# Kernel tuning notes

Measured on AMD Instinct MI355X. Metric: run time of the kernel, lower is better.

Reference implementation:

```python
import jax, jax.numpy as jnp
import numpy as np

N = 50000      # nodes
E = 800000     # edges (before self loops)
G = 64         # graphs in batch
F_IN = 11
HID = 64
C = 8
NEG_SLOPE = 0.2


def setup_inputs() -> dict:
    key = jax.random.key(0)
    ks = jax.random.split(key, 20)
    inp = {
        "x": jax.random.normal(ks[0], (N, F_IN), dtype=jnp.float32),
        "edge_index": jax.random.randint(ks[1], (2, E), 0, N, dtype=jnp.int64),
        "edge_attr": jax.random.normal(ks[2], (E, 17), dtype=jnp.float32),
        "batch": jnp.sort(jax.random.randint(ks[3], (N,), 0, G, dtype=jnp.int64)),
    }
    def glorot(k, shape):
        fan_in, fan_out = shape[0], shape[-1]
        s = jnp.sqrt(6.0 / (fan_in + fan_out))
        return jax.random.uniform(k, shape, jnp.float32, -s, s)
    # GATConv layers (heads=1): W [in,out], att vectors a_src/a_dst [out], bias [out]
    inp["W1"] = glorot(ks[4], (F_IN, HID)); inp["a1s"] = glorot(ks[5], (HID,)); inp["a1d"] = glorot(ks[6], (HID,)); inp["b1"] = jnp.zeros((HID,), jnp.float32)
    inp["W2"] = glorot(ks[7], (HID, HID)); inp["a2s"] = glorot(ks[8], (HID,)); inp["a2d"] = glorot(ks[9], (HID,)); inp["b2"] = jnp.zeros((HID,), jnp.float32)
    inp["W3"] = glorot(ks[10], (HID, C)); inp["a3s"] = glorot(ks[11], (C,)); inp["a3d"] = glorot(ks[12], (C,)); inp["b3"] = jnp.zeros((C,), jnp.float32)
    return inp


def _gat_layer(x, src, dst, W, a_s, a_d, b):
    # x: [N,in] -> h: [N,out]; single head, concat irrelevant for heads=1
    h = x @ W
    alpha_src = h @ a_s            # [N]
    alpha_dst = h @ a_d            # [N]
    e = jax.nn.leaky_relu(alpha_src[src] + alpha_dst[dst], negative_slope=NEG_SLOPE)  # [E']
    # segment-wise (per destination node) softmax over incoming edges
    m = jax.ops.segment_max(e, dst, num_segments=N)
    ex = jnp.exp(e - m[dst])
    denom = jax.ops.segment_sum(ex, dst, num_segments=N)
    alpha = ex / denom[dst]
    out = jax.ops.segment_sum(alpha[:, None] * h[src], dst, num_segments=N)
    return out + b


def reference(x, edge_index, edge_attr, batch, W1, a1s, a1d, b1, W2, a2s, a2d, b2, W3, a3s, a3d, b3):
    del edge_attr  # GATConv without edge_dim ignores edge_attr
    loop = jnp.arange(N, dtype=edge_index.dtype)
    src = jnp.concatenate([edge_index[0], loop])  # add self loops
    dst = jnp.concatenate([edge_index[1], loop])
    h = jax.nn.relu(_gat_layer(x, src, dst, W1, a1s, a1d, b1))
    h = jax.nn.relu(_gat_layer(h, src, dst, W2, a2s, a2d, b2))
    h = jax.nn.relu(_gat_layer(h, src, dst, W3, a3s, a3d, b3))
    # global mean pool over graphs
    counts = jax.ops.segment_sum(jnp.ones((N,), h.dtype), batch, num_segments=G)
    pooled = jax.ops.segment_sum(h, batch, num_segments=G) / jnp.maximum(counts, 1.0)[:, None]
    # dropout is identity in eval mode
    return jax.nn.sigmoid(pooled)
```

## Files before the change

kernel.cpp:

```cpp
#include <hip/hip_runtime.h>

#define NN 50000
#define EE 800000
#define GG 64
#define CC 8

#define NBKT 196
#define NCHK 782
#define CHUNK 1024
#define CAP 8192
#define NB4G 12500

__device__ unsigned g_done = 0;

__device__ __forceinline__ float lrelu(float z) { return fmaxf(z, 0.2f * z); }
__device__ __forceinline__ unsigned short f2bf(float v) {
    unsigned u = __float_as_uint(v);
    return (unsigned short)((u + 0x7FFFu + ((u >> 16) & 1u)) >> 16);
}
__device__ __forceinline__ float bf2f(unsigned short b) {
    return __uint_as_float(((unsigned)b) << 16);
}
__device__ __forceinline__ float2 bf2x2(unsigned d) {
    float2 r;
    r.x = __uint_as_float(d << 16);
    r.y = __uint_as_float(d & 0xFFFF0000u);
    return r;
}


__global__ __launch_bounds__(256) void k0_mm11_hist(const float* __restrict__ x, const float* __restrict__ W,
                                                    const float* __restrict__ avs, const float* __restrict__ avd,
                                                    unsigned short* __restrict__ h, float* __restrict__ as_,
                                                    float* __restrict__ ad_, const int* __restrict__ dst,
                                                    int* __restrict__ G) {
    __shared__ float xT[11 * 68];
    __shared__ float Wl[11 * 64];
    __shared__ float avl[64], adl[64];
    __shared__ int hist[NBKT];
    int t = threadIdx.x;
    int nbase = blockIdx.x * 64;
    for (int idx = t; idx < 11 * 64; idx += 256) Wl[idx] = W[idx];
    if (t < 64) { avl[t] = avs[t]; adl[t] = avd[t]; }
    for (int idx = t; idx < 64 * 11; idx += 256) {
        int n = idx / 11, k = idx - n * 11;
        int gn = nbase + n;
        if (gn >= NN) gn = NN - 1;
        xT[k * 68 + n] = x[gn * 11 + k];
    }
    for (int i = t; i < NBKT; i += 256) hist[i] = 0;
    __syncthreads();
    int f0 = (t & 15) * 4;
    int n0 = (t >> 4) * 4;
    float a00=0,a01=0,a02=0,a03=0, a10=0,a11=0,a12=0,a13=0;
    float a20=0,a21=0,a22=0,a23=0, a30=0,a31=0,a32=0,a33=0;
#pragma unroll
    for (int k = 0; k < 11; k++) {
        float4 xv = *(const float4*)&xT[k * 68 + n0];
        float4 wv = *(const float4*)&Wl[k * 64 + f0];
        a00 += xv.x * wv.x; a01 += xv.x * wv.y; a02 += xv.x * wv.z; a03 += xv.x * wv.w;
        a10 += xv.y * wv.x; a11 += xv.y * wv.y; a12 += xv.y * wv.z; a13 += xv.y * wv.w;
        a20 += xv.z * wv.x; a21 += xv.z * wv.y; a22 += xv.z * wv.z; a23 += xv.z * wv.w;
        a30 += xv.w * wv.x; a31 += xv.w * wv.y; a32 += xv.w * wv.z; a33 += xv.w * wv.w;
    }
    float4 av = *(const float4*)&avl[f0];
    float4 dv = *(const float4*)&adl[f0];
    float vs[4], vd[4];
    vs[0] = a00*av.x + a01*av.y + a02*av.z + a03*av.w;
    vs[1] = a10*av.x + a11*av.y + a12*av.z + a13*av.w;
    vs[2] = a20*av.x + a21*av.y + a22*av.z + a23*av.w;
    vs[3] = a30*av.x + a31*av.y + a32*av.z + a33*av.w;
    vd[0] = a00*dv.x + a01*dv.y + a02*dv.z + a03*dv.w;
    vd[1] = a10*dv.x + a11*dv.y + a12*dv.z + a13*dv.w;
    vd[2] = a20*dv.x + a21*dv.y + a22*dv.z + a23*dv.w;
    vd[3] = a30*dv.x + a31*dv.y + a32*dv.z + a33*dv.w;
#pragma unroll
    for (int o = 1; o < 16; o <<= 1) {
#pragma unroll
        for (int ni = 0; ni < 4; ni++) {
            vs[ni] += __shfl_xor(vs[ni], o);
            vd[ni] += __shfl_xor(vd[ni], o);
        }
    }
    ushort4* h4 = (ushort4*)h;
    int nn0 = nbase + n0;
    float rows[4][4] = {{a00,a01,a02,a03},{a10,a11,a12,a13},{a20,a21,a22,a23},{a30,a31,a32,a33}};
#pragma unroll
    for (int ni = 0; ni < 4; ni++) {
        if (nn0 + ni < NN) {
            ushort4 pv;
            pv.x = f2bf(rows[ni][0]); pv.y = f2bf(rows[ni][1]);
            pv.z = f2bf(rows[ni][2]); pv.w = f2bf(rows[ni][3]);
            h4[(nn0 + ni) * 16 + (t & 15)] = pv;
            if ((t & 15) == 0) { as_[nn0 + ni] = vs[ni]; ad_[nn0 + ni] = vd[ni]; }
        }
    }
    int e0 = blockIdx.x * CHUNK;
    int e1 = min(e0 + CHUNK, EE);
    for (int e = e0 + t; e < e1; e += 256) atomicAdd(&hist[dst[e] >> 8], 1);
    __syncthreads();
    for (int i = t; i < NBKT; i += 256) G[blockIdx.x * NBKT + i] = hist[i];
}


__global__ __launch_bounds__(256) void k1_scan(const int* __restrict__ G, int* __restrict__ offs,
                                               int* __restrict__ bT, float* __restrict__ pool,
                                               float* __restrict__ cntf, int* __restrict__ rowptr) {
    __shared__ int s[256];
    int t = threadIdx.x, j = blockIdx.x;
    int c0 = t * 4;
    int v0 = (c0 + 0 < NCHK) ? G[(c0 + 0) * NBKT + j] : 0;
    int v1 = (c0 + 1 < NCHK) ? G[(c0 + 1) * NBKT + j] : 0;
    int v2 = (c0 + 2 < NCHK) ? G[(c0 + 2) * NBKT + j] : 0;
    int v3 = (c0 + 3 < NCHK) ? G[(c0 + 3) * NBKT + j] : 0;
    int tsum = v0 + v1 + v2 + v3;
    s[t] = tsum;
    __syncthreads();
#pragma unroll
    for (int off = 1; off < 256; off <<= 1) {
        int u = (t >= off) ? s[t - off] : 0;
        __syncthreads();
        s[t] += u;
        __syncthreads();
    }
    int excl = s[t] - tsum;
    if (c0 + 0 < NCHK) offs[(c0 + 0) * NBKT + j] = excl;
    if (c0 + 1 < NCHK) offs[(c0 + 1) * NBKT + j] = excl + v0;
    if (c0 + 2 < NCHK) offs[(c0 + 2) * NBKT + j] = excl + v0 + v1;
    if (c0 + 3 < NCHK) offs[(c0 + 3) * NBKT + j] = excl + v0 + v1 + v2;
    if (t == 255) bT[j] = s[255];
    if (j == 0) {
        for (int i = t; i < GG * CC; i += 256) pool[i] = 0.f;
        if (t < GG) cntf[t] = 0.f;
        if (t == 0) rowptr[NN] = EE;
    }
}


__global__ __launch_bounds__(256) void k2_part(const int* __restrict__ src, const int* __restrict__ dst,
                                               const int* __restrict__ offs, const int* __restrict__ bT,
                                               unsigned* __restrict__ pairs) {
    __shared__ int s[256];
    __shared__ int bst[NBKT];
    __shared__ int cur[NBKT];
    int t = threadIdx.x, c = blockIdx.x;
    int v = (t < NBKT) ? bT[t] : 0;
    s[t] = v;
    __syncthreads();
#pragma unroll
    for (int off = 1; off < 256; off <<= 1) {
        int u = (t >= off) ? s[t - off] : 0;
        __syncthreads();
        s[t] += u;
        __syncthreads();
    }
    if (t < NBKT) bst[t] = s[t] - v;
    __syncthreads();
    for (int i = t; i < NBKT; i += 256) cur[i] = bst[i] + offs[c * NBKT + i];
    __syncthreads();
    int e0 = c * CHUNK, e1 = min(e0 + CHUNK, EE);
    for (int e = e0 + t; e < e1; e += 256) {
        int d = dst[e];
        int pos = atomicAdd(&cur[d >> 8], 1);
        pairs[pos] = (unsigned)src[e] | ((unsigned)(d & 255) << 16);
    }
}


__global__ __launch_bounds__(256) void k3_sort(const unsigned* __restrict__ pairs, const int* __restrict__ bT,
                                               int* __restrict__ col, int* __restrict__ rowptr) {
    __shared__ unsigned pL[CAP];
    __shared__ int hist[256];
    __shared__ int sc[256];
    int t = threadIdx.x, j = blockIdx.x;
    int v = (t < NBKT) ? bT[t] : 0;
    hist[t] = v;
    __syncthreads();
#pragma unroll
    for (int off = 1; off < 256; off <<= 1) {
        int u = (t >= off) ? hist[t - off] : 0;
        __syncthreads();
        hist[t] += u;
        __syncthreads();
    }
    if (t == j) { sc[0] = hist[t] - v; sc[1] = v; }
    __syncthreads();
    int start = sc[0];
    int cnt = sc[1];
    if (cnt > CAP) cnt = CAP;
    int nb = j * 256;
    int nodeCnt = min(256, NN - nb);
    __syncthreads();
    hist[t] = 0;
    __syncthreads();
    for (int i = t; i < cnt; i += 256) {
        unsigned p = pairs[start + i];
        pL[i] = p;
        atomicAdd(&hist[p >> 16], 1);
    }
    __syncthreads();
    int c2 = hist[t];
    sc[t] = c2;
    __syncthreads();
#pragma unroll
    for (int off = 1; off < 256; off <<= 1) {
        int u = (t >= off) ? sc[t - off] : 0;
        __syncthreads();
        sc[t] += u;
        __syncthreads();
    }
    int excl = sc[t] - c2;
    if (t < nodeCnt) rowptr[nb + t] = start + excl;
    hist[t] = excl;
    __syncthreads();
    for (int i = t; i < cnt; i += 256) {
        unsigned p = pL[i];
        int pos = atomicAdd(&hist[p >> 16], 1);
        col[start + pos] = (int)(p & 0xFFFFu);
    }
}


__global__ __launch_bounds__(256) void k_mm64t(const unsigned short* __restrict__ xin,
                                               const float* __restrict__ W,
                                               const float* __restrict__ avs, const float* __restrict__ avd,
                                               unsigned short* __restrict__ h, float* __restrict__ as_,
                                               float* __restrict__ ad_) {
    __shared__ float xT[64 * 68];
    __shared__ float Wl[64 * 64];
    __shared__ float avl[64], adl[64];
    int t = threadIdx.x;
    int nbase = blockIdx.x * 64;
    for (int idx = t; idx < 64 * 64; idx += 256) Wl[idx] = W[idx];
    if (t < 64) { avl[t] = avs[t]; adl[t] = avd[t]; }
    for (int idx = t; idx < 64 * 64; idx += 256) {
        int n = idx / 64, k = idx - n * 64;
        int gn = nbase + n;
        if (gn >= NN) gn = NN - 1;
        xT[k * 68 + n] = bf2f(xin[gn * 64 + k]);
    }
    __syncthreads();
    int f0 = (t & 15) * 4;
    int n0 = (t >> 4) * 4;
    float a00=0,a01=0,a02=0,a03=0, a10=0,a11=0,a12=0,a13=0;
    float a20=0,a21=0,a22=0,a23=0, a30=0,a31=0,a32=0,a33=0;
#pragma unroll 4
    for (int k = 0; k < 64; k++) {
        float4 xv = *(const float4*)&xT[k * 68 + n0];
        float4 wv = *(const float4*)&Wl[k * 64 + f0];
        a00 += xv.x * wv.x; a01 += xv.x * wv.y; a02 += xv.x * wv.z; a03 += xv.x * wv.w;
        a10 += xv.y * wv.x; a11 += xv.y * wv.y; a12 += xv.y * wv.z; a13 += xv.y * wv.w;
        a20 += xv.z * wv.x; a21 += xv.z * wv.y; a22 += xv.z * wv.z; a23 += xv.z * wv.w;
        a30 += xv.w * wv.x; a31 += xv.w * wv.y; a32 += xv.w * wv.z; a33 += xv.w * wv.w;
    }
    float4 av = *(const float4*)&avl[f0];
    float4 dv = *(const float4*)&adl[f0];
    float vs[4], vd[4];
    vs[0] = a00*av.x + a01*av.y + a02*av.z + a03*av.w;
    vs[1] = a10*av.x + a11*av.y + a12*av.z + a13*av.w;
    vs[2] = a20*av.x + a21*av.y + a22*av.z + a23*av.w;
    vs[3] = a30*av.x + a31*av.y + a32*av.z + a33*av.w;
    vd[0] = a00*dv.x + a01*dv.y + a02*dv.z + a03*dv.w;
    vd[1] = a10*dv.x + a11*dv.y + a12*dv.z + a13*dv.w;
    vd[2] = a20*dv.x + a21*dv.y + a22*dv.z + a23*dv.w;
    vd[3] = a30*dv.x + a31*dv.y + a32*dv.z + a33*dv.w;
#pragma unroll
    for (int o = 1; o < 16; o <<= 1) {
#pragma unroll
        for (int ni = 0; ni < 4; ni++) {
            vs[ni] += __shfl_xor(vs[ni], o);
            vd[ni] += __shfl_xor(vd[ni], o);
        }
    }
    ushort4* h4 = (ushort4*)h;
    int nn0 = nbase + n0;
    float rows[4][4] = {{a00,a01,a02,a03},{a10,a11,a12,a13},{a20,a21,a22,a23},{a30,a31,a32,a33}};
#pragma unroll
    for (int ni = 0; ni < 4; ni++) {
        if (nn0 + ni < NN) {
            ushort4 pv;
            pv.x = f2bf(rows[ni][0]); pv.y = f2bf(rows[ni][1]);
            pv.z = f2bf(rows[ni][2]); pv.w = f2bf(rows[ni][3]);
            h4[(nn0 + ni) * 16 + (t & 15)] = pv;
            if ((t & 15) == 0) { as_[nn0 + ni] = vs[ni]; ad_[nn0 + ni] = vd[ni]; }
        }
    }
}


template <bool FUSE>
__global__ __launch_bounds__(256) void k_agg64(const unsigned short* __restrict__ h,
                                               const int* __restrict__ rowptr,
                                               const int* __restrict__ col, const float* __restrict__ as_,
                                               const float* __restrict__ ad_, const float* __restrict__ bias,
                                               unsigned short* __restrict__ out16,
                                               const float* __restrict__ W3, const float* __restrict__ a3s,
                                               const float* __restrict__ a3d,
                                               float* __restrict__ as3, float* __restrict__ ad3) {
    __shared__ float W3p[64 * 9];
    if constexpr (FUSE) {
        for (int idx = threadIdx.x; idx < 512; idx += 256)
            W3p[(idx >> 3) * 9 + (idx & 7)] = W3[idx];
        __syncthreads();
    }
    int wid = threadIdx.x >> 6;
    int node = blockIdx.x * 4 + wid;
    int lane = threadIdx.x & 63;
    int rp0 = rowptr[node];
    int deg = rowptr[node + 1] - rp0;
    float adn = ad_[node];
    float zself = lrelu(as_[node] + adn);
    const uint4* hb4 = (const uint4*)h;
    int f = lane & 7, eg = lane >> 3;
    float acc[8] = {0.f, 0.f, 0.f, 0.f, 0.f, 0.f, 0.f, 0.f};
    if (deg <= 32) {
        uint4 rowreg[4];
        float zk[4];
#pragma unroll
        for (int k = 0; k < 4; k++) {
            int e = k * 8 + eg;
            zk[k] = -1e30f;
            if (e < deg) {
                int se = col[rp0 + e];
                zk[k] = lrelu(as_[se] + adn);
                rowreg[k] = hb4[se * 8 + f];
            }
        }
        float M = fmaxf(fmaxf(zk[0], zk[1]), fmaxf(zk[2], zk[3]));
#pragma unroll
        for (int o = 8; o <= 32; o <<= 1) M = fmaxf(M, __shfl_xor(M, o));
        M = fmaxf(M, zself);
        float s0 = 0.f;
#pragma unroll
        for (int k = 0; k < 4; k++) { zk[k] = __expf(zk[k] - M); s0 += zk[k]; }
        float exs = __expf(zself - M);
        float sum = s0;
#pragma unroll
        for (int o = 8; o <= 32; o <<= 1) sum += __shfl_xor(sum, o);
        float inv = 1.f / (sum + exs);
#pragma unroll
        for (int k = 0; k < 4; k++) {
            int e = k * 8 + eg;
            if (e < deg) {
                float w = zk[k] * inv;
                float2 p0 = bf2x2(rowreg[k].x), p1 = bf2x2(rowreg[k].y);
                float2 p2 = bf2x2(rowreg[k].z), p3 = bf2x2(rowreg[k].w);
                acc[0] += w * p0.x; acc[1] += w * p0.y;
                acc[2] += w * p1.x; acc[3] += w * p1.y;
                acc[4] += w * p2.x; acc[5] += w * p2.y;
                acc[6] += w * p3.x; acc[7] += w * p3.y;
            }
        }
        if (eg == 0) {
            float w0 = exs * inv;
            uint4 hv = hb4[node * 8 + f];
            float2 p0 = bf2x2(hv.x), p1 = bf2x2(hv.y), p2 = bf2x2(hv.z), p3 = bf2x2(hv.w);
            acc[0] += w0 * p0.x; acc[1] += w0 * p0.y;
            acc[2] += w0 * p1.x; acc[3] += w0 * p1.y;
            acc[4] += w0 * p2.x; acc[5] += w0 * p2.y;
            acc[6] += w0 * p3.x; acc[7] += w0 * p3.y;
        }
    } else {
        float m = -1e30f, l = 0.f;
        for (int i = lane; i < deg; i += 64) {
            float z = lrelu(as_[col[rp0 + i]] + adn);
            float mn = fmaxf(m, z);
            l = l * __expf(m - mn) + __expf(z - mn);
            m = mn;
        }
        if (lane == 0) {
            float mn = fmaxf(m, zself);
            l = l * __expf(m - mn) + __expf(zself - mn);
            m = mn;
        }
#pragma unroll
        for (int o = 32; o; o >>= 1) {
            float mo = __shfl_xor(m, o), lo = __shfl_xor(l, o);
            float mn = fmaxf(m, mo);
            l = l * __expf(m - mn) + lo * __expf(mo - mn);
            m = mn;
        }
        float Em = m;
        float inv = 1.f / l;
        for (int base = 0; base < deg; base += 8) {
            int i = base + eg;
            if (i < deg) {
                int sv = col[rp0 + i];
                float al = __expf(lrelu(as_[sv] + adn) - Em) * inv;
                uint4 hv = hb4[sv * 8 + f];
                float2 p0 = bf2x2(hv.x), p1 = bf2x2(hv.y), p2 = bf2x2(hv.z), p3 = bf2x2(hv.w);
                acc[0] += al * p0.x; acc[1] += al * p0.y;
                acc[2] += al * p1.x; acc[3] += al * p1.y;
                acc[4] += al * p2.x; acc[5] += al * p2.y;
                acc[6] += al * p3.x; acc[7] += al * p3.y;
            }
        }
        if (eg == 0) {
            float al = __expf(zself - Em) * inv;
            uint4 hv = hb4[node * 8 + f];
            float2 p0 = bf2x2(hv.x), p1 = bf2x2(hv.y), p2 = bf2x2(hv.z), p3 = bf2x2(hv.w);
            acc[0] += al * p0.x; acc[1] += al * p0.y;
            acc[2] += al * p1.x; acc[3] += al * p1.y;
            acc[4] += al * p2.x; acc[5] += al * p2.y;
            acc[6] += al * p3.x; acc[7] += al * p3.y;
        }
    }
#pragma unroll
    for (int o = 8; o <= 32; o <<= 1) {
#pragma unroll
        for (int j = 0; j < 8; j++) acc[j] += __shfl_xor(acc[j], o);
    }
    float4 b0 = ((const float4*)bias)[2 * f];
    float4 b1 = ((const float4*)bias)[2 * f + 1];
    float r[8];
    r[0] = fmaxf(acc[0] + b0.x, 0.f); r[1] = fmaxf(acc[1] + b0.y, 0.f);
    r[2] = fmaxf(acc[2] + b0.z, 0.f); r[3] = fmaxf(acc[3] + b0.w, 0.f);
    r[4] = fmaxf(acc[4] + b1.x, 0.f); r[5] = fmaxf(acc[5] + b1.y, 0.f);
    r[6] = fmaxf(acc[6] + b1.z, 0.f); r[7] = fmaxf(acc[7] + b1.w, 0.f);
    if constexpr (!FUSE) {
        if (eg == 0) {
            uint4 pv;
            pv.x = (unsigned)f2bf(r[0]) | ((unsigned)f2bf(r[1]) << 16);
            pv.y = (unsigned)f2bf(r[2]) | ((unsigned)f2bf(r[3]) << 16);
            pv.z = (unsigned)f2bf(r[4]) | ((unsigned)f2bf(r[5]) << 16);
            pv.w = (unsigned)f2bf(r[6]) | ((unsigned)f2bf(r[7]) << 16);
            ((uint4*)out16)[node * 8 + f] = pv;
        }
    } else {
        float p = 0.f;
#pragma unroll
        for (int i = 0; i < 8; i++) p += r[i] * W3p[(f * 8 + i) * 9 + eg];
#pragma unroll
        for (int o = 1; o < 8; o <<= 1) p += __shfl_xor(p, o);
        float vs = p * a3s[eg];
        float vd = p * a3d[eg];
#pragma unroll
        for (int o = 8; o <= 32; o <<= 1) { vs += __shfl_xor(vs, o); vd += __shfl_xor(vd, o); }
        if (lane == 0) { as3[node] = vs; ad3[node] = vd; }
        if (f == 0) out16[node * 8 + eg] = f2bf(p);
    }
}


__global__ __launch_bounds__(256) void k_agg8(const unsigned short* __restrict__ h,
                                              const int* __restrict__ rowptr,
                                              const int* __restrict__ col, const float* __restrict__ as_,
                                              const float* __restrict__ ad_, const float* __restrict__ bias,
                                              float* __restrict__ out) {
    int wid = threadIdx.x >> 6;
    int node = blockIdx.x * 4 + wid;
    int lane = threadIdx.x & 63;
    int rp0 = rowptr[node];
    int deg = rowptr[node + 1] - rp0;
    float adn = ad_[node];
    float zself = lrelu(as_[node] + adn);
    const uint2* h2 = (const uint2*)h;
    int f = lane & 1, eg = lane >> 1;
    float acc[4] = {0.f, 0.f, 0.f, 0.f};
    if (deg <= 32) {
        float z = -1e30f;
        uint2 rr = make_uint2(0u, 0u);
        if (eg < deg) {
            int se = col[rp0 + eg];
            z = lrelu(as_[se] + adn);
            rr = h2[se * 2 + f];
        }
        float M = z;
#pragma unroll
        for (int o = 2; o <= 32; o <<= 1) M = fmaxf(M, __shfl_xor(M, o));
        M = fmaxf(M, zself);
        float ex = __expf(z - M);
        float exs = __expf(zself - M);
        float sum = ex;
#pragma unroll
        for (int o = 2; o <= 32; o <<= 1) sum += __shfl_xor(sum, o);
        float inv = 1.f / (sum + exs);
        float w = ex * inv;
        float2 lo = bf2x2(rr.x), hi = bf2x2(rr.y);
        acc[0] = w * lo.x; acc[1] = w * lo.y; acc[2] = w * hi.x; acc[3] = w * hi.y;
        if (eg == 0) {
            float w0 = exs * inv;
            uint2 hv = h2[node * 2 + f];
            float2 l2 = bf2x2(hv.x), h2v = bf2x2(hv.y);
            acc[0] += w0 * l2.x; acc[1] += w0 * l2.y;
            acc[2] += w0 * h2v.x; acc[3] += w0 * h2v.y;
        }
    } else {
        float m = -1e30f, l = 0.f;
        for (int i = lane; i < deg; i += 64) {
            float z = lrelu(as_[col[rp0 + i]] + adn);
            float mn = fmaxf(m, z);
            l = l * __expf(m - mn) + __expf(z - mn);
            m = mn;
        }
        if (lane == 0) {
            float mn = fmaxf(m, zself);
            l = l * __expf(m - mn) + __expf(zself - mn);
            m = mn;
        }
#pragma unroll
        for (int o = 32; o; o >>= 1) {
            float mo = __shfl_xor(m, o), lo = __shfl_xor(l, o);
            float mn = fmaxf(m, mo);
            l = l * __expf(m - mn) + lo * __expf(mo - mn);
            m = mn;
        }
        float Em = m;
        float inv = 1.f / l;
        for (int base = 0; base < deg; base += 32) {
            int i = base + eg;
            if (i < deg) {
                int sv = col[rp0 + i];
                float al = __expf(lrelu(as_[sv] + adn) - Em) * inv;
                uint2 hv = h2[sv * 2 + f];
                float2 lo = bf2x2(hv.x), hi = bf2x2(hv.y);
                acc[0] += al * lo.x; acc[1] += al * lo.y;
                acc[2] += al * hi.x; acc[3] += al * hi.y;
            }
        }
        if (eg == 0) {
            float al = __expf(zself - Em) * inv;
            uint2 hv = h2[node * 2 + f];
            float2 lo = bf2x2(hv.x), hi = bf2x2(hv.y);
            acc[0] += al * lo.x; acc[1] += al * lo.y;
            acc[2] += al * hi.x; acc[3] += al * hi.y;
        }
    }
#pragma unroll
    for (int o = 2; o <= 32; o <<= 1) {
#pragma unroll
        for (int j = 0; j < 4; j++) acc[j] += __shfl_xor(acc[j], o);
    }
    if (eg == 0) {
        float4 bv = ((const float4*)bias)[f];
        float4 o4;
        o4.x = fmaxf(acc[0] + bv.x, 0.f);
        o4.y = fmaxf(acc[1] + bv.y, 0.f);
        o4.z = fmaxf(acc[2] + bv.z, 0.f);
        o4.w = fmaxf(acc[3] + bv.w, 0.f);
        ((float4*)out)[node * 2 + f] = o4;
    }
}


__global__ __launch_bounds__(256) void k9_poolfinal(const float* __restrict__ h3, const int* __restrict__ batch,
                                                    float* __restrict__ pool, float* __restrict__ cntf,
                                                    float* __restrict__ out) {
    __shared__ float pl[GG * CC + GG];
    __shared__ int lastFlag;
    int t = threadIdx.x;
    for (int idx = t; idx < GG * CC + GG; idx += 256) pl[idx] = 0.f;
    __syncthreads();
    int node = blockIdx.x * 256 + t;
    if (node < NN) {
        int g = batch[node];
#pragma unroll
        for (int c = 0; c < CC; c++) atomicAdd(&pl[g * CC + c], h3[node * CC + c]);
        atomicAdd(&pl[GG * CC + g], 1.0f);
    }
    __syncthreads();
    for (int idx = t; idx < GG * CC + GG; idx += 256) {
        float v = pl[idx];
        if (idx < GG * CC)
            atomicAdd(&pool[idx], v);
        else
            atomicAdd(&cntf[idx - GG * CC], v);
    }
    __syncthreads();
    if (t == 0) {
        __threadfence();
        unsigned r = __hip_atomic_fetch_add(&g_done, 1u, __ATOMIC_ACQ_REL, __HIP_MEMORY_SCOPE_AGENT);
        lastFlag = (r == (unsigned)(NBKT - 1));
    }
    __syncthreads();
    if (lastFlag) {
        __threadfence();
        for (int i = t; i < GG * CC; i += 256) {
            int g = i >> 3;
            float c = __hip_atomic_load(&cntf[g], __ATOMIC_RELAXED, __HIP_MEMORY_SCOPE_AGENT);
            float p = __hip_atomic_load(&pool[i], __ATOMIC_RELAXED, __HIP_MEMORY_SCOPE_AGENT);
            float v = p / fmaxf(c, 1.0f);
            out[i] = 1.0f / (1.0f + __expf(-v));
        }
        if (t == 0)
            __hip_atomic_store(&g_done, 0u, __ATOMIC_RELAXED, __HIP_MEMORY_SCOPE_AGENT);
    }
}


extern "C" void kernel_launch(void* const* d_in, const int* in_sizes, int n_in,
                              void* d_out, int out_size, void* d_ws, size_t ws_size,
                              hipStream_t stream) {
    const float* x   = (const float*)d_in[0];
    const int*   ei  = (const int*)d_in[1];
    const int*   bat = (const int*)d_in[3];
    const float* W1  = (const float*)d_in[4];
    const float* a1s = (const float*)d_in[5];
    const float* a1d = (const float*)d_in[6];
    const float* b1  = (const float*)d_in[7];
    const float* W2  = (const float*)d_in[8];
    const float* a2s = (const float*)d_in[9];
    const float* a2d = (const float*)d_in[10];
    const float* b2  = (const float*)d_in[11];
    const float* W3  = (const float*)d_in[12];
    const float* a3s = (const float*)d_in[13];
    const float* a3d = (const float*)d_in[14];
    const float* b3  = (const float*)d_in[15];
    float* out = (float*)d_out;

    float* fb = (float*)d_ws;
    unsigned short* hA16 = (unsigned short*)fb;
    unsigned short* hB16 = (unsigned short*)(fb + NN * 32);
    unsigned short* h316 = (unsigned short*)(fb + NN * 64);
    float* h3b  = fb + NN * 64 + NN * 4;
    float* as_  = h3b + NN * 8;
    float* ad_  = as_ + NN;
    float* as3  = ad_ + NN;
    float* ad3  = as3 + NN;
    int* rowptr = (int*)(ad3 + NN);
    int* col    = rowptr + NN + 1;
    int* G      = col + EE;
    int* offs   = G + NCHK * NBKT;
    int* bT     = offs + NCHK * NBKT;
    unsigned* pairs = (unsigned*)(bT + 256);
    float* pool = (float*)(pairs + EE);
    float* cntf = pool + GG * CC;

    const int NB64 = (NN + 63) / 64;

    const int* srcE = ei;
    const int* dstE = ei + EE;

    k0_mm11_hist<<<NB64, 256, 0, stream>>>(x, W1, a1s, a1d, hA16, as_, ad_, dstE, G);
    k1_scan<<<NBKT, 256, 0, stream>>>(G, offs, bT, pool, cntf, rowptr);
    k2_part<<<NCHK, 256, 0, stream>>>(srcE, dstE, offs, bT, pairs);
    k3_sort<<<NBKT, 256, 0, stream>>>(pairs, bT, col, rowptr);

    k_agg64<false><<<NB4G, 256, 0, stream>>>(hA16, rowptr, col, as_, ad_, b1, hB16,
                                             nullptr, nullptr, nullptr, nullptr, nullptr);
    k_mm64t<<<NB64, 256, 0, stream>>>(hB16, W2, a2s, a2d, hA16, as_, ad_);
    k_agg64<true><<<NB4G, 256, 0, stream>>>(hA16, rowptr, col, as_, ad_, b2, h316,
                                            W3, a3s, a3d, as3, ad3);
    k_agg8<<<NB4G, 256, 0, stream>>>(h316, rowptr, col, as3, ad3, b3, h3b);
    k9_poolfinal<<<NBKT, 256, 0, stream>>>(h3b, bat, pool, cntf, out);
}
```

Measured before the change: 268.6 us.

## Build CSR with per-node global atomic counts and direct scatter instead of bucket sort

Replaces the two-level bucket partition plus in-LDS sort with a simpler CSR build. Per-destination counts come from global atomics, then a two-pass block scan and a global-atomic scatter of source indices into col. This drops the pairs buffer, the per-chunk histogram matrix and the LDS sort kernel. In exchange it adds heavy contended global atomics and a non-deterministic edge order within each row, which can change floating-point summation order.

Result: slower. 324.8 us (+20.9%).

```diff
diff --git a/kernel.cpp b/kernel.cpp
--- a/kernel.cpp
+++ b/kernel.cpp
@@ -8,8 +8,8 @@
 #define NBKT 196
 #define NCHK 782
 #define CHUNK 1024
-#define CAP 8192
 #define NB4G 12500
+#define NBE  3125
 
 __device__ unsigned g_done = 0;
 
@@ -29,15 +29,25 @@
 }
 
 
+__global__ __launch_bounds__(256) void k_init(int* __restrict__ cnt, float* __restrict__ pool,
+                                              float* __restrict__ cntf) {
+    int n = blockIdx.x * 256 + threadIdx.x;
+    if (n < NN) cnt[n] = 0;
+    if (blockIdx.x == 0) {
+        for (int i = threadIdx.x; i < GG * CC; i += 256) pool[i] = 0.f;
+        if (threadIdx.x < GG) cntf[threadIdx.x] = 0.f;
+    }
+}
+
+
 __global__ __launch_bounds__(256) void k0_mm11_hist(const float* __restrict__ x, const float* __restrict__ W,
                                                     const float* __restrict__ avs, const float* __restrict__ avd,
                                                     unsigned short* __restrict__ h, float* __restrict__ as_,
                                                     float* __restrict__ ad_, const int* __restrict__ dst,
-                                                    int* __restrict__ G) {
+                                                    int* __restrict__ cnt) {
     __shared__ float xT[11 * 68];
     __shared__ float Wl[11 * 64];
     __shared__ float avl[64], adl[64];
-    __shared__ int hist[NBKT];
     int t = threadIdx.x;
     int nbase = blockIdx.x * 64;
     for (int idx = t; idx < 11 * 64; idx += 256) Wl[idx] = W[idx];
@@ -48,7 +58,6 @@
         if (gn >= NN) gn = NN - 1;
         xT[k * 68 + n] = x[gn * 11 + k];
     }
-    for (int i = t; i < NBKT; i += 256) hist[i] = 0;
     __syncthreads();
     int f0 = (t & 15) * 4;
     int n0 = (t >> 4) * 4;
@@ -97,24 +106,17 @@
     }
     int e0 = blockIdx.x * CHUNK;
     int e1 = min(e0 + CHUNK, EE);
-    for (int e = e0 + t; e < e1; e += 256) atomicAdd(&hist[dst[e] >> 8], 1);
-    __syncthreads();
-    for (int i = t; i < NBKT; i += 256) G[blockIdx.x * NBKT + i] = hist[i];
-}
-
-
-__global__ __launch_bounds__(256) void k1_scan(const int* __restrict__ G, int* __restrict__ offs,
-                                               int* __restrict__ bT, float* __restrict__ pool,
-                                               float* __restrict__ cntf, int* __restrict__ rowptr) {
+    for (int e = e0 + t; e < e1; e += 256) atomicAdd(&cnt[dst[e]], 1);
+}
+
+
+__global__ __launch_bounds__(256) void k1a_scan(const int* __restrict__ cnt, int* __restrict__ rowptr,
+                                                int* __restrict__ bsum) {
     __shared__ int s[256];
     int t = threadIdx.x, j = blockIdx.x;
-    int c0 = t * 4;
-    int v0 = (c0 + 0 < NCHK) ? G[(c0 + 0) * NBKT + j] : 0;
-    int v1 = (c0 + 1 < NCHK) ? G[(c0 + 1) * NBKT + j] : 0;
-    int v2 = (c0 + 2 < NCHK) ? G[(c0 + 2) * NBKT + j] : 0;
-    int v3 = (c0 + 3 < NCHK) ? G[(c0 + 3) * NBKT + j] : 0;
-    int tsum = v0 + v1 + v2 + v3;
-    s[t] = tsum;
+    int n = j * 256 + t;
+    int v = (n < NN) ? cnt[n] : 0;
+    s[t] = v;
     __syncthreads();
 #pragma unroll
     for (int off = 1; off < 256; off <<= 1) {
@@ -123,100 +125,39 @@
         s[t] += u;
         __syncthreads();
     }
-    int excl = s[t] - tsum;
-    if (c0 + 0 < NCHK) offs[(c0 + 0) * NBKT + j] = excl;
-    if (c0 + 1 < NCHK) offs[(c0 + 1) * NBKT + j] = excl + v0;
-    if (c0 + 2 < NCHK) offs[(c0 + 2) * NBKT + j] = excl + v0 + v1;
-    if (c0 + 3 < NCHK) offs[(c0 + 3) * NBKT + j] = excl + v0 + v1 + v2;
-    if (t == 255) bT[j] = s[255];
-    if (j == 0) {
-        for (int i = t; i < GG * CC; i += 256) pool[i] = 0.f;
-        if (t < GG) cntf[t] = 0.f;
-        if (t == 0) rowptr[NN] = EE;
-    }
-}
-
-
-__global__ __launch_bounds__(256) void k2_part(const int* __restrict__ src, const int* __restrict__ dst,
-                                               const int* __restrict__ offs, const int* __restrict__ bT,
-                                               unsigned* __restrict__ pairs) {
+    if (n < NN) rowptr[n] = s[t] - v;
+    if (t == 255) bsum[j] = s[255];
+}
+
+__global__ __launch_bounds__(256) void k1b_add(int* __restrict__ rowptr, const int* __restrict__ bsum,
+                                               int* __restrict__ cursor) {
     __shared__ int s[256];
-    __shared__ int bst[NBKT];
-    __shared__ int cur[NBKT];
-    int t = threadIdx.x, c = blockIdx.x;
-    int v = (t < NBKT) ? bT[t] : 0;
-    s[t] = v;
-    __syncthreads();
-#pragma unroll
-    for (int off = 1; off < 256; off <<= 1) {
-        int u = (t >= off) ? s[t - off] : 0;
+    int t = threadIdx.x, j = blockIdx.x;
+    s[t] = (t < j) ? bsum[t] : 0;
+    __syncthreads();
+#pragma unroll
+    for (int off = 128; off; off >>= 1) {
+        if (t < off) s[t] += s[t + off];
         __syncthreads();
-        s[t] += u;
-        __syncthreads();
-    }
-    if (t < NBKT) bst[t] = s[t] - v;
-    __syncthreads();
-    for (int i = t; i < NBKT; i += 256) cur[i] = bst[i] + offs[c * NBKT + i];
-    __syncthreads();
-    int e0 = c * CHUNK, e1 = min(e0 + CHUNK, EE);
-    for (int e = e0 + t; e < e1; e += 256) {
+    }
+    int offset = s[0];
+    int n = j * 256 + t;
+    if (n < NN) {
+        int r = rowptr[n] + offset;
+        rowptr[n] = r;
+        cursor[n] = r;
+    }
+    if (j == 0 && t == 0) rowptr[NN] = EE;
+}
+
+
+__global__ __launch_bounds__(256) void k2s_scatter(const int* __restrict__ src, const int* __restrict__ dst,
+                                                   int* __restrict__ cursor, int* __restrict__ col) {
+    int e = blockIdx.x * 256 + threadIdx.x;
+    if (e < EE) {
         int d = dst[e];
-        int pos = atomicAdd(&cur[d >> 8], 1);
-        pairs[pos] = (unsigned)src[e] | ((unsigned)(d & 255) << 16);
-    }
-}
-
-
-__global__ __launch_bounds__(256) void k3_sort(const unsigned* __restrict__ pairs, const int* __restrict__ bT,
-                                               int* __restrict__ col, int* __restrict__ rowptr) {
-    __shared__ unsigned pL[CAP];
-    __shared__ int hist[256];
-    __shared__ int sc[256];
-    int t = threadIdx.x, j = blockIdx.x;
-    int v = (t < NBKT) ? bT[t] : 0;
-    hist[t] = v;
-    __syncthreads();
-#pragma unroll
-    for (int off = 1; off < 256; off <<= 1) {
-        int u = (t >= off) ? hist[t - off] : 0;
-        __syncthreads();
-        hist[t] += u;
-        __syncthreads();
-    }
-    if (t == j) { sc[0] = hist[t] - v; sc[1] = v; }
-    __syncthreads();
-    int start = sc[0];
-    int cnt = sc[1];
-    if (cnt > CAP) cnt = CAP;
-    int nb = j * 256;
-    int nodeCnt = min(256, NN - nb);
-    __syncthreads();
-    hist[t] = 0;
-    __syncthreads();
-    for (int i = t; i < cnt; i += 256) {
-        unsigned p = pairs[start + i];
-        pL[i] = p;
-        atomicAdd(&hist[p >> 16], 1);
-    }
-    __syncthreads();
-    int c2 = hist[t];
-    sc[t] = c2;
-    __syncthreads();
-#pragma unroll
-    for (int off = 1; off < 256; off <<= 1) {
-        int u = (t >= off) ? sc[t - off] : 0;
-        __syncthreads();
-        sc[t] += u;
-        __syncthreads();
-    }
-    int excl = sc[t] - c2;
-    if (t < nodeCnt) rowptr[nb + t] = start + excl;
-    hist[t] = excl;
-    __syncthreads();
-    for (int i = t; i < cnt; i += 256) {
-        unsigned p = pL[i];
-        int pos = atomicAdd(&hist[p >> 16], 1);
-        col[start + pos] = (int)(p & 0xFFFFu);
+        int pos = atomicAdd(&cursor[d], 1);
+        col[pos] = src[e];
     }
 }
 
@@ -619,11 +560,10 @@
     float* ad3  = as3 + NN;
     int* rowptr = (int*)(ad3 + NN);
     int* col    = rowptr + NN + 1;
-    int* G      = col + EE;
-    int* offs   = G + NCHK * NBKT;
-    int* bT     = offs + NCHK * NBKT;
-    unsigned* pairs = (unsigned*)(bT + 256);
-    float* pool = (float*)(pairs + EE);
+    int* cnt    = col + EE;
+    int* cursor = cnt + NN;
+    int* bsum   = cursor + NN;
+    float* pool = (float*)(bsum + 256);
     float* cntf = pool + GG * CC;
 
     const int NB64 = (NN + 63) / 64;
@@ -631,10 +571,11 @@
     const int* srcE = ei;
     const int* dstE = ei + EE;
 
-    k0_mm11_hist<<<NB64, 256, 0, stream>>>(x, W1, a1s, a1d, hA16, as_, ad_, dstE, G);
-    k1_scan<<<NBKT, 256, 0, stream>>>(G, offs, bT, pool, cntf, rowptr);
-    k2_part<<<NCHK, 256, 0, stream>>>(srcE, dstE, offs, bT, pairs);
-    k3_sort<<<NBKT, 256, 0, stream>>>(pairs, bT, col, rowptr);
+    k_init<<<NBKT, 256, 0, stream>>>(cnt, pool, cntf);
+    k0_mm11_hist<<<NB64, 256, 0, stream>>>(x, W1, a1s, a1d, hA16, as_, ad_, dstE, cnt);
+    k1a_scan<<<NBKT, 256, 0, stream>>>(cnt, rowptr, bsum);
+    k1b_add<<<NBKT, 256, 0, stream>>>(rowptr, bsum, cursor);
+    k2s_scatter<<<NBE, 256, 0, stream>>>(srcE, dstE, cursor, col);
 
     k_agg64<false><<<NB4G, 256, 0, stream>>>(hA16, rowptr, col, as_, ad_, b1, hB16,
                                              nullptr, nullptr, nullptr, nullptr, nullptr);
```

## Fuse layer-2 linear transform into layer-1 aggregation epilogue

Applied to the files above, without the earlier changes.

Removes the standalone 64x64 matmul kernel and computes h@W2 plus the attention logits inside the layer-1 aggregation kernel, once each node's aggregated row is ready. The intermediate bf16 activation no longer makes a separate write-then-read round trip, and one launch is dropped. In exchange, each block stages a transposed 64x66 W2 tile in shared memory. Each wavefront also does extra FMAs and shuffle reductions per node, which may lower occupancy and lengthen the aggregation kernel. Separate as2/ad2 buffers are added so the next layer does not read the logits being overwritten.

Result: slower. 309.1 us (+15.1%).

```diff
diff --git a/kernel.cpp b/kernel.cpp
--- a/kernel.cpp
+++ b/kernel.cpp
@@ -221,91 +221,34 @@
 }
 
 
-__global__ __launch_bounds__(256) void k_mm64t(const unsigned short* __restrict__ xin,
-                                               const float* __restrict__ W,
-                                               const float* __restrict__ avs, const float* __restrict__ avd,
-                                               unsigned short* __restrict__ h, float* __restrict__ as_,
-                                               float* __restrict__ ad_) {
-    __shared__ float xT[64 * 68];
-    __shared__ float Wl[64 * 64];
-    __shared__ float avl[64], adl[64];
-    int t = threadIdx.x;
-    int nbase = blockIdx.x * 64;
-    for (int idx = t; idx < 64 * 64; idx += 256) Wl[idx] = W[idx];
-    if (t < 64) { avl[t] = avs[t]; adl[t] = avd[t]; }
-    for (int idx = t; idx < 64 * 64; idx += 256) {
-        int n = idx / 64, k = idx - n * 64;
-        int gn = nbase + n;
-        if (gn >= NN) gn = NN - 1;
-        xT[k * 68 + n] = bf2f(xin[gn * 64 + k]);
-    }
-    __syncthreads();
-    int f0 = (t & 15) * 4;
-    int n0 = (t >> 4) * 4;
-    float a00=0,a01=0,a02=0,a03=0, a10=0,a11=0,a12=0,a13=0;
-    float a20=0,a21=0,a22=0,a23=0, a30=0,a31=0,a32=0,a33=0;
-#pragma unroll 4
-    for (int k = 0; k < 64; k++) {
-        float4 xv = *(const float4*)&xT[k * 68 + n0];
-        float4 wv = *(const float4*)&Wl[k * 64 + f0];
-        a00 += xv.x * wv.x; a01 += xv.x * wv.y; a02 += xv.x * wv.z; a03 += xv.x * wv.w;
-        a10 += xv.y * wv.x; a11 += xv.y * wv.y; a12 += xv.y * wv.z; a13 += xv.y * wv.w;
-        a20 += xv.z * wv.x; a21 += xv.z * wv.y; a22 += xv.z * wv.z; a23 += xv.z * wv.w;
-        a30 += xv.w * wv.x; a31 += xv.w * wv.y; a32 += xv.w * wv.z; a33 += xv.w * wv.w;
-    }
-    float4 av = *(const float4*)&avl[f0];
-    float4 dv = *(const float4*)&adl[f0];
-    float vs[4], vd[4];
-    vs[0] = a00*av.x + a01*av.y + a02*av.z + a03*av.w;
-    vs[1] = a10*av.x + a11*av.y + a12*av.z + a13*av.w;
-    vs[2] = a20*av.x + a21*av.y + a22*av.z + a23*av.w;
-    vs[3] = a30*av.x + a31*av.y + a32*av.z + a33*av.w;
-    vd[0] = a00*dv.x + a01*dv.y + a02*dv.z + a03*dv.w;
-    vd[1] = a10*dv.x + a11*dv.y + a12*dv.z + a13*dv.w;
-    vd[2] = a20*dv.x + a21*dv.y + a22*dv.z + a23*dv.w;
-    vd[3] = a30*dv.x + a31*dv.y + a32*dv.z + a33*dv.w;
-#pragma unroll
-    for (int o = 1; o < 16; o <<= 1) {
-#pragma unroll
-        for (int ni = 0; ni < 4; ni++) {
-            vs[ni] += __shfl_xor(vs[ni], o);
-            vd[ni] += __shfl_xor(vd[ni], o);
-        }
-    }
-    ushort4* h4 = (ushort4*)h;
-    int nn0 = nbase + n0;
-    float rows[4][4] = {{a00,a01,a02,a03},{a10,a11,a12,a13},{a20,a21,a22,a23},{a30,a31,a32,a33}};
-#pragma unroll
-    for (int ni = 0; ni < 4; ni++) {
-        if (nn0 + ni < NN) {
-            ushort4 pv;
-            pv.x = f2bf(rows[ni][0]); pv.y = f2bf(rows[ni][1]);
-            pv.z = f2bf(rows[ni][2]); pv.w = f2bf(rows[ni][3]);
-            h4[(nn0 + ni) * 16 + (t & 15)] = pv;
-            if ((t & 15) == 0) { as_[nn0 + ni] = vs[ni]; ad_[nn0 + ni] = vd[ni]; }
-        }
-    }
-}
-
-
-template <bool FUSE>
+template <int MODE>
 __global__ __launch_bounds__(256) void k_agg64(const unsigned short* __restrict__ h,
                                                const int* __restrict__ rowptr,
                                                const int* __restrict__ col, const float* __restrict__ as_,
                                                const float* __restrict__ ad_, const float* __restrict__ bias,
                                                unsigned short* __restrict__ out16,
-                                               const float* __restrict__ W3, const float* __restrict__ a3s,
-                                               const float* __restrict__ a3d,
-                                               float* __restrict__ as3, float* __restrict__ ad3) {
-    __shared__ float W3p[64 * 9];
-    if constexpr (FUSE) {
-        for (int idx = threadIdx.x; idx < 512; idx += 256)
-            W3p[(idx >> 3) * 9 + (idx & 7)] = W3[idx];
-        __syncthreads();
-    }
-    int wid = threadIdx.x >> 6;
+                                               const float* __restrict__ Wx, const float* __restrict__ axs,
+                                               const float* __restrict__ axd,
+                                               float* __restrict__ asN, float* __restrict__ adN) {
+    __shared__ float WL[MODE == 1 ? 64 * 66 : 64 * 9];
+    __shared__ float avl2[MODE == 1 ? 64 : 1];
+    __shared__ float adl2[MODE == 1 ? 64 : 1];
+    int t = threadIdx.x;
+    if constexpr (MODE == 1) {
+        for (int idx = t; idx < 4096; idx += 256) {
+            int k = idx >> 6, j = idx & 63;
+            WL[j * 66 + k] = Wx[idx];
+        }
+        if (t < 64) { avl2[t] = axs[t]; adl2[t] = axd[t]; }
+        __syncthreads();
+    } else {
+        for (int idx = t; idx < 512; idx += 256)
+            WL[(idx >> 3) * 9 + (idx & 7)] = Wx[idx];
+        __syncthreads();
+    }
+    int wid = t >> 6;
     int node = blockIdx.x * 4 + wid;
-    int lane = threadIdx.x & 63;
+    int lane = t & 63;
     int rp0 = rowptr[node];
     int deg = rowptr[node + 1] - rp0;
     float adn = ad_[node];
@@ -417,26 +360,52 @@
     r[2] = fmaxf(acc[2] + b0.z, 0.f); r[3] = fmaxf(acc[3] + b0.w, 0.f);
     r[4] = fmaxf(acc[4] + b1.x, 0.f); r[5] = fmaxf(acc[5] + b1.y, 0.f);
     r[6] = fmaxf(acc[6] + b1.z, 0.f); r[7] = fmaxf(acc[7] + b1.w, 0.f);
-    if constexpr (!FUSE) {
-        if (eg == 0) {
+    if constexpr (MODE == 1) {
+        float P[8];
+#pragma unroll
+        for (int jj = 0; jj < 8; jj++) {
+            const float* wrow = &WL[(8 * eg + jj) * 66 + 8 * f];
+            float p = 0.f;
+#pragma unroll
+            for (int i2 = 0; i2 < 4; i2++) {
+                float2 w = *(const float2*)&wrow[2 * i2];
+                p += r[2 * i2] * w.x + r[2 * i2 + 1] * w.y;
+            }
+            P[jj] = p;
+        }
+#pragma unroll
+        for (int o = 1; o < 8; o <<= 1) {
+#pragma unroll
+            for (int jj = 0; jj < 8; jj++) P[jj] += __shfl_xor(P[jj], o);
+        }
+        float vsp = 0.f, vdp = 0.f;
+#pragma unroll
+        for (int jj = 0; jj < 8; jj++) {
+            vsp += P[jj] * avl2[8 * eg + jj];
+            vdp += P[jj] * adl2[8 * eg + jj];
+        }
+#pragma unroll
+        for (int o = 8; o <= 32; o <<= 1) { vsp += __shfl_xor(vsp, o); vdp += __shfl_xor(vdp, o); }
+        if (lane == 0) { asN[node] = vsp; adN[node] = vdp; }
+        if (f == 0) {
             uint4 pv;
-            pv.x = (unsigned)f2bf(r[0]) | ((unsigned)f2bf(r[1]) << 16);
-            pv.y = (unsigned)f2bf(r[2]) | ((unsigned)f2bf(r[3]) << 16);
-            pv.z = (unsigned)f2bf(r[4]) | ((unsigned)f2bf(r[5]) << 16);
-            pv.w = (unsigned)f2bf(r[6]) | ((unsigned)f2bf(r[7]) << 16);
-            ((uint4*)out16)[node * 8 + f] = pv;
+            pv.x = (unsigned)f2bf(P[0]) | ((unsigned)f2bf(P[1]) << 16);
+            pv.y = (unsigned)f2bf(P[2]) | ((unsigned)f2bf(P[3]) << 16);
+            pv.z = (unsigned)f2bf(P[4]) | ((unsigned)f2bf(P[5]) << 16);
+            pv.w = (unsigned)f2bf(P[6]) | ((unsigned)f2bf(P[7]) << 16);
+            ((uint4*)out16)[node * 8 + eg] = pv;
         }
     } else {
         float p = 0.f;
 #pragma unroll
-        for (int i = 0; i < 8; i++) p += r[i] * W3p[(f * 8 + i) * 9 + eg];
+        for (int i = 0; i < 8; i++) p += r[i] * WL[(f * 8 + i) * 9 + eg];
 #pragma unroll
         for (int o = 1; o < 8; o <<= 1) p += __shfl_xor(p, o);
-        float vs = p * a3s[eg];
-        float vd = p * a3d[eg];
+        float vs = p * axs[eg];
+        float vd = p * axd[eg];
 #pragma unroll
         for (int o = 8; o <= 32; o <<= 1) { vs += __shfl_xor(vs, o); vd += __shfl_xor(vd, o); }
-        if (lane == 0) { as3[node] = vs; ad3[node] = vd; }
+        if (lane == 0) { asN[node] = vs; adN[node] = vd; }
         if (f == 0) out16[node * 8 + eg] = f2bf(p);
     }
 }
@@ -615,7 +584,9 @@
     float* h3b  = fb + NN * 64 + NN * 4;
     float* as_  = h3b + NN * 8;
     float* ad_  = as_ + NN;
-    float* as3  = ad_ + NN;
+    float* as2  = ad_ + NN;
+    float* ad2  = as2 + NN;
+    float* as3  = ad2 + NN;
     float* ad3  = as3 + NN;
     int* rowptr = (int*)(ad3 + NN);
     int* col    = rowptr + NN + 1;
@@ -636,11 +607,10 @@
     k2_part<<<NCHK, 256, 0, stream>>>(srcE, dstE, offs, bT, pairs);
     k3_sort<<<NBKT, 256, 0, stream>>>(pairs, bT, col, rowptr);
 
-    k_agg64<false><<<NB4G, 256, 0, stream>>>(hA16, rowptr, col, as_, ad_, b1, hB16,
-                                             nullptr, nullptr, nullptr, nullptr, nullptr);
-    k_mm64t<<<NB64, 256, 0, stream>>>(hB16, W2, a2s, a2d, hA16, as_, ad_);
-    k_agg64<true><<<NB4G, 256, 0, stream>>>(hA16, rowptr, col, as_, ad_, b2, h316,
-                                            W3, a3s, a3d, as3, ad3);
+    k_agg64<1><<<NB4G, 256, 0, stream>>>(hA16, rowptr, col, as_, ad_, b1, hB16,
+                                         W2, a2s, a2d, as2, ad2);
+    k_agg64<2><<<NB4G, 256, 0, stream>>>(hB16, rowptr, col, as2, ad2, b2, h316,
+                                         W3, a3s, a3d, as3, ad3);
     k_agg8<<<NB4G, 256, 0, stream>>>(h316, rowptr, col, as3, ad3, b3, h3b);
     k9_poolfinal<<<NBKT, 256, 0, stream>>>(h3b, bat, pool, cntf, out);
 }
```

## Use 64-node buckets in CSR build and hoist bucket-start scan to own kernel

Applied to the files above, without the earlier changes.

Shrinks the counting-sort buckets from 256 to 64 destination nodes, giving 782 buckets instead of 196. The local sort kernel now runs 782 blocks with a smaller shared buffer, and each block no longer rescans the bucket totals itself. A new single-block kernel computes bucket start offsets once, and the partition and sort kernels read them. This raises parallelism and occupancy in the sort stage at the cost of an extra launch, a larger histogram matrix, and the capacity dropping to 4096 edges per bucket.

Measured after the change: 279.1 us. 1.04x slower.

```diff
diff --git a/kernel.cpp b/kernel.cpp
--- a/kernel.cpp
+++ b/kernel.cpp
@@ -6,9 +6,10 @@
 #define CC 8
 
 #define NBKT 196
+#define NBK2 782
 #define NCHK 782
 #define CHUNK 1024
-#define CAP 8192
+#define CAP 4096
 #define NB4G 12500
 
 __device__ unsigned g_done = 0;
@@ -37,7 +38,7 @@
     __shared__ float xT[11 * 68];
     __shared__ float Wl[11 * 64];
     __shared__ float avl[64], adl[64];
-    __shared__ int hist[NBKT];
+    __shared__ int hist[NBK2];
     int t = threadIdx.x;
     int nbase = blockIdx.x * 64;
     for (int idx = t; idx < 11 * 64; idx += 256) Wl[idx] = W[idx];
@@ -48,7 +49,7 @@
         if (gn >= NN) gn = NN - 1;
         xT[k * 68 + n] = x[gn * 11 + k];
     }
-    for (int i = t; i < NBKT; i += 256) hist[i] = 0;
+    for (int i = t; i < NBK2; i += 256) hist[i] = 0;
     __syncthreads();
     int f0 = (t & 15) * 4;
     int n0 = (t >> 4) * 4;
@@ -97,9 +98,9 @@
     }
     int e0 = blockIdx.x * CHUNK;
     int e1 = min(e0 + CHUNK, EE);
-    for (int e = e0 + t; e < e1; e += 256) atomicAdd(&hist[dst[e] >> 8], 1);
-    __syncthreads();
-    for (int i = t; i < NBKT; i += 256) G[blockIdx.x * NBKT + i] = hist[i];
+    for (int e = e0 + t; e < e1; e += 256) atomicAdd(&hist[dst[e] >> 6], 1);
+    __syncthreads();
+    for (int i = t; i < NBK2; i += 256) G[blockIdx.x * NBK2 + i] = hist[i];
 }
 
 
@@ -109,10 +110,10 @@
     __shared__ int s[256];
     int t = threadIdx.x, j = blockIdx.x;
     int c0 = t * 4;
-    int v0 = (c0 + 0 < NCHK) ? G[(c0 + 0) * NBKT + j] : 0;
-    int v1 = (c0 + 1 < NCHK) ? G[(c0 + 1) * NBKT + j] : 0;
-    int v2 = (c0 + 2 < NCHK) ? G[(c0 + 2) * NBKT + j] : 0;
-    int v3 = (c0 + 3 < NCHK) ? G[(c0 + 3) * NBKT + j] : 0;
+    int v0 = (c0 + 0 < NCHK) ? G[(c0 + 0) * NBK2 + j] : 0;
+    int v1 = (c0 + 1 < NCHK) ? G[(c0 + 1) * NBK2 + j] : 0;
+    int v2 = (c0 + 2 < NCHK) ? G[(c0 + 2) * NBK2 + j] : 0;
+    int v3 = (c0 + 3 < NCHK) ? G[(c0 + 3) * NBK2 + j] : 0;
     int tsum = v0 + v1 + v2 + v3;
     s[t] = tsum;
     __syncthreads();
@@ -124,10 +125,10 @@
         __syncthreads();
     }
     int excl = s[t] - tsum;
-    if (c0 + 0 < NCHK) offs[(c0 + 0) * NBKT + j] = excl;
-    if (c0 + 1 < NCHK) offs[(c0 + 1) * NBKT + j] = excl + v0;
-    if (c0 + 2 < NCHK) offs[(c0 + 2) * NBKT + j] = excl + v0 + v1;
-    if (c0 + 3 < NCHK) offs[(c0 + 3) * NBKT + j] = excl + v0 + v1 + v2;
+    if (c0 + 0 < NCHK) offs[(c0 + 0) * NBK2 + j] = excl;
+    if (c0 + 1 < NCHK) offs[(c0 + 1) * NBK2 + j] = excl + v0;
+    if (c0 + 2 < NCHK) offs[(c0 + 2) * NBK2 + j] = excl + v0 + v1;
+    if (c0 + 3 < NCHK) offs[(c0 + 3) * NBK2 + j] = excl + v0 + v1 + v2;
     if (t == 255) bT[j] = s[255];
     if (j == 0) {
         for (int i = t; i < GG * CC; i += 256) pool[i] = 0.f;
@@ -137,15 +138,16 @@
 }
 
 
-__global__ __launch_bounds__(256) void k2_part(const int* __restrict__ src, const int* __restrict__ dst,
-                                               const int* __restrict__ offs, const int* __restrict__ bT,
-                                               unsigned* __restrict__ pairs) {
+__global__ __launch_bounds__(256) void k1c_bstart(const int* __restrict__ bT, int* __restrict__ bstart) {
     __shared__ int s[256];
-    __shared__ int bst[NBKT];
-    __shared__ int cur[NBKT];
-    int t = threadIdx.x, c = blockIdx.x;
-    int v = (t < NBKT) ? bT[t] : 0;
-    s[t] = v;
+    int t = threadIdx.x;
+    int c0 = t * 4;
+    int v0 = (c0 + 0 < NBK2) ? bT[c0 + 0] : 0;
+    int v1 = (c0 + 1 < NBK2) ? bT[c0 + 1] : 0;
+    int v2 = (c0 + 2 < NBK2) ? bT[c0 + 2] : 0;
+    int v3 = (c0 + 3 < NBK2) ? bT[c0 + 3] : 0;
+    int tsum = v0 + v1 + v2 + v3;
+    s[t] = tsum;
     __syncthreads();
 #pragma unroll
     for (int off = 1; off < 256; off <<= 1) {
@@ -154,44 +156,43 @@
         s[t] += u;
         __syncthreads();
     }
-    if (t < NBKT) bst[t] = s[t] - v;
-    __syncthreads();
-    for (int i = t; i < NBKT; i += 256) cur[i] = bst[i] + offs[c * NBKT + i];
+    int excl = s[t] - tsum;
+    if (c0 + 0 < NBK2) bstart[c0 + 0] = excl;
+    if (c0 + 1 < NBK2) bstart[c0 + 1] = excl + v0;
+    if (c0 + 2 < NBK2) bstart[c0 + 2] = excl + v0 + v1;
+    if (c0 + 3 < NBK2) bstart[c0 + 3] = excl + v0 + v1 + v2;
+    if (t == 255) bstart[NBK2] = s[255];
+}
+
+
+__global__ __launch_bounds__(256) void k2_part(const int* __restrict__ src, const int* __restrict__ dst,
+                                               const int* __restrict__ offs, const int* __restrict__ bstart,
+                                               unsigned* __restrict__ pairs) {
+    __shared__ int cur[NBK2];
+    int t = threadIdx.x, c = blockIdx.x;
+    for (int i = t; i < NBK2; i += 256) cur[i] = bstart[i] + offs[c * NBK2 + i];
     __syncthreads();
     int e0 = c * CHUNK, e1 = min(e0 + CHUNK, EE);
     for (int e = e0 + t; e < e1; e += 256) {
         int d = dst[e];
-        int pos = atomicAdd(&cur[d >> 8], 1);
-        pairs[pos] = (unsigned)src[e] | ((unsigned)(d & 255) << 16);
-    }
-}
-
-
-__global__ __launch_bounds__(256) void k3_sort(const unsigned* __restrict__ pairs, const int* __restrict__ bT,
+        int pos = atomicAdd(&cur[d >> 6], 1);
+        pairs[pos] = (unsigned)src[e] | ((unsigned)(d & 63) << 16);
+    }
+}
+
+
+__global__ __launch_bounds__(256) void k3_sort(const unsigned* __restrict__ pairs, const int* __restrict__ bstart,
                                                int* __restrict__ col, int* __restrict__ rowptr) {
     __shared__ unsigned pL[CAP];
-    __shared__ int hist[256];
-    __shared__ int sc[256];
+    __shared__ int hist[64];
+    __shared__ int sc[64];
     int t = threadIdx.x, j = blockIdx.x;
-    int v = (t < NBKT) ? bT[t] : 0;
-    hist[t] = v;
-    __syncthreads();
-#pragma unroll
-    for (int off = 1; off < 256; off <<= 1) {
-        int u = (t >= off) ? hist[t - off] : 0;
-        __syncthreads();
-        hist[t] += u;
-        __syncthreads();
-    }
-    if (t == j) { sc[0] = hist[t] - v; sc[1] = v; }
-    __syncthreads();
-    int start = sc[0];
-    int cnt = sc[1];
+    int start = bstart[j];
+    int cnt = bstart[j + 1] - start;
     if (cnt > CAP) cnt = CAP;
-    int nb = j * 256;
-    int nodeCnt = min(256, NN - nb);
-    __syncthreads();
-    hist[t] = 0;
+    int nb = j * 64;
+    int nodeCnt = min(64, NN - nb);
+    if (t < 64) hist[t] = 0;
     __syncthreads();
     for (int i = t; i < cnt; i += 256) {
         unsigned p = pairs[start + i];
@@ -199,19 +200,19 @@
         atomicAdd(&hist[p >> 16], 1);
     }
     __syncthreads();
-    int c2 = hist[t];
-    sc[t] = c2;
-    __syncthreads();
-#pragma unroll
-    for (int off = 1; off < 256; off <<= 1) {
-        int u = (t >= off) ? sc[t - off] : 0;
+    int c2 = (t < 64) ? hist[t] : 0;
+    if (t < 64) sc[t] = c2;
+    __syncthreads();
+#pragma unroll
+    for (int off = 1; off < 64; off <<= 1) {
+        int u = (t >= off && t < 64) ? sc[t - off] : 0;
         __syncthreads();
-        sc[t] += u;
+        if (t < 64) sc[t] += u;
         __syncthreads();
     }
-    int excl = sc[t] - c2;
+    int excl = (t < 64) ? (sc[t] - c2) : 0;
     if (t < nodeCnt) rowptr[nb + t] = start + excl;
-    hist[t] = excl;
+    if (t < 64) hist[t] = excl;
     __syncthreads();
     for (int i = t; i < cnt; i += 256) {
         unsigned p = pL[i];
@@ -620,9 +621,10 @@
     int* rowptr = (int*)(ad3 + NN);
     int* col    = rowptr + NN + 1;
     int* G      = col + EE;
-    int* offs   = G + NCHK * NBKT;
-    int* bT     = offs + NCHK * NBKT;
-    unsigned* pairs = (unsigned*)(bT + 256);
+    int* offs   = G + NCHK * NBK2;
+    int* bT     = offs + NCHK * NBK2;
+    int* bstart = bT + 1024;
+    unsigned* pairs = (unsigned*)(bstart + 1024);
     float* pool = (float*)(pairs + EE);
     float* cntf = pool + GG * CC;
 
@@ -632,9 +634,10 @@
     const int* dstE = ei + EE;
 
     k0_mm11_hist<<<NB64, 256, 0, stream>>>(x, W1, a1s, a1d, hA16, as_, ad_, dstE, G);
-    k1_scan<<<NBKT, 256, 0, stream>>>(G, offs, bT, pool, cntf, rowptr);
-    k2_part<<<NCHK, 256, 0, stream>>>(srcE, dstE, offs, bT, pairs);
-    k3_sort<<<NBKT, 256, 0, stream>>>(pairs, bT, col, rowptr);
+    k1_scan<<<NBK2, 256, 0, stream>>>(G, offs, bT, pool, cntf, rowptr);
+    k1c_bstart<<<1, 256, 0, stream>>>(bT, bstart);
+    k2_part<<<NCHK, 256, 0, stream>>>(srcE, dstE, offs, bstart, pairs);
+    k3_sort<<<NBK2, 256, 0, stream>>>(pairs, bstart, col, rowptr);
 
     k_agg64<false><<<NB4G, 256, 0, stream>>>(hA16, rowptr, col, as_, ad_, b1, hB16,
                                              nullptr, nullptr, nullptr, nullptr, nullptr);
```
